# Kernel tuning notes

Hardware: AMD Instinct MI355X
Metric: run time of the kernel (lower is better)

## Reference

```python
import jax, jax.numpy as jnp
import numpy as np

FRAC_BIT = 12
SCALE = float(2 ** FRAC_BIT)          # 12 fractional bits
QMIN, QMAX = -32768.0, 32767.0        # signed 16-bit two's complement range


def quant16(x):
    """Quantize to signed 16-bit fixed point with 12 fractional bits.

    Matches float_to_16bits_tensor / bit_slice semantics: the bit-serial
    crossbar MVM of the sliced operands equals an exact integer product of
    these fixed-point values, rescaled back to float.
    """
    return jnp.clip(jnp.round(x * SCALE), QMIN, QMAX) / SCALE


def setup_inputs() -> dict:
    key = jax.random.key(0)
    k1, k2 = jax.random.split(key)
    x = jax.random.normal(k1, (32, 128, 56, 56), dtype=jnp.float32)
    # kaiming-ish scale so weights are well inside the fixed-point range
    weight = jax.random.normal(k2, (256, 128, 3, 3), dtype=jnp.float32) * 0.05
    return {"x": x, "weight": weight}


def reference(x, weight):
    # The nested i/j loop in the original slides a stride-1 window over the
    # zero-padded input, performing a bit-sliced crossbar MVM per pixel.
    # That is exactly conv2d(stride=1, padding=1) on 16-bit fixed-point
    # quantized input and weight (bias row in the crossbar is zero / unused).
    qx = quant16(x)
    qw = quant16(weight)
    out = jax.lax.conv_general_dilated(
        qx, qw,
        window_strides=(1, 1),
        padding=((1, 1), (1, 1)),
        dimension_numbers=("NCHW", "OIHW", "NCHW"),
    )
    return out
```

## Files before the change

kernel.cpp:

```cpp
#include <hip/hip_runtime.h>
#include <cstdint>
#include <cstddef>


typedef __attribute__((ext_vector_type(8))) short short8;
typedef __attribute__((ext_vector_type(4))) float floatx4;

#define NIMG 32
#define CIN  128
#define HW   56
#define KOUT 256
#define HP   58
#define XPAD_ELEMS ((size_t)NIMG * HP * HP * CIN)
#define WT_OFF_BYTES (XPAD_ELEMS * 2)
#define KK 1152

__device__ __forceinline__ uint16_t quant_bf16(float v) {
    float q = rintf(v * 4096.0f);
    q = fminf(fmaxf(q, -32768.0f), 32767.0f) * (1.0f / 4096.0f);
    union { float f; uint32_t u; } cv; cv.f = q;
    uint32_t u = cv.u;
    return (uint16_t)((u + 0x7fffu + ((u >> 16) & 1u)) >> 16);
}

__global__ __launch_bounds__(256) void quant_pad_x(const float* __restrict__ x,
                                                   uint16_t* __restrict__ xp) {
    const int b = blockIdx.x;
    const int n = b / HP, hp = b - n * HP;
    uint16_t* row = xp + (size_t)(n * HP + hp) * HP * CIN;

    if (hp == 0 || hp == HP - 1) {
        uint4 z{0, 0, 0, 0};
        uint4* d = (uint4*)row;
        for (int t = threadIdx.x; t < HP * CIN * 2 / 16; t += 256) d[t] = z;
        return;
    }
    const int h = hp - 1;
    __shared__ uint16_t tile[HW * 130];
    const float* src = x + (size_t)n * CIN * HW * HW + (size_t)h * HW;
    for (int t = threadIdx.x; t < CIN * 14; t += 256) {
        int c = t / 14, w4 = t - c * 14;
        float4 v = *(const float4*)(src + (size_t)c * (HW * HW) + w4 * 4);
        int base = (w4 * 4) * 130 + c;
        tile[base]       = quant_bf16(v.x);
        tile[base + 130] = quant_bf16(v.y);
        tile[base + 260] = quant_bf16(v.z);
        tile[base + 390] = quant_bf16(v.w);
    }
    __syncthreads();
    if (threadIdx.x < 32) {
        uint4 z{0, 0, 0, 0};
        if (threadIdx.x < 16) ((uint4*)row)[threadIdx.x] = z;
        else ((uint4*)(row + 57 * CIN))[threadIdx.x - 16] = z;
    }
    uint2* dst = (uint2*)(row + CIN);
    for (int t = threadIdx.x; t < (HW * CIN) / 4; t += 256) {
        int w = t >> 5, c4 = (t & 31) * 4;
        uint32_t a = tile[w * 130 + c4]     | ((uint32_t)tile[w * 130 + c4 + 1] << 16);
        uint32_t c = tile[w * 130 + c4 + 2] | ((uint32_t)tile[w * 130 + c4 + 3] << 16);
        dst[t] = make_uint2(a, c);
    }
}

__global__ __launch_bounds__(256) void quant_w(const float* __restrict__ w,
                                               uint16_t* __restrict__ wt) {
    int i = blockIdx.x * 256 + threadIdx.x;
    int k = i / KK;
    int r = i - k * KK;
    int tap = r >> 7;
    int c = r & 127;
    wt[i] = quant_bf16(w[(size_t)(k * CIN + c) * 9 + tap]);
}

__global__ __launch_bounds__(256) void conv_gemm(const uint16_t* __restrict__ xp,
                                                 const uint16_t* __restrict__ wt,
                                                 float* __restrict__ out) {
    __shared__ __align__(16) uint16_t As[128 * 64];
    __shared__ __align__(16) uint16_t Bs[128 * 64];

    const int tid = threadIdx.x;
    const int l   = tid & 63;
    const int wv  = tid >> 6;
    const int wr  = wv >> 1;
    const int wc  = wv & 1;
    const int kblk  = blockIdx.x;
    const int pxblk = blockIdx.y;

    const int srow   = l >> 3;
    const int c_data = (l & 7) ^ srow;

    const uint16_t* aG[4];
    const uint16_t* bG[4];
#pragma unroll
    for (int i = 0; i < 4; ++i) {
        int row = wv * 32 + i * 8 + srow;
        aG[i] = wt + (size_t)(kblk * 128 + row) * KK + c_data * 8;
        int p = pxblk * 128 + row;
        int n = p / 3136; int rem = p - n * 3136;
        int hh = rem / HW; int ww = rem - hh * HW;
        bG[i] = xp + (size_t)((n * HP + hh) * HP + ww) * CIN + c_data * 8;
    }

    floatx4 acc[4][4];
#pragma unroll
    for (int a = 0; a < 4; ++a)
#pragma unroll
        for (int b = 0; b < 4; ++b)
            acc[a][b] = (floatx4){0.f, 0.f, 0.f, 0.f};

    const int m16 = l & 15;
    const int q   = l >> 4;
    const int r7  = m16 & 7;

    for (int tap = 0; tap < 9; ++tap) {
        const int toff = ((tap / 3) * HP + (tap % 3)) * CIN;
#pragma unroll
        for (int c64 = 0; c64 < 2; ++c64) {
            const int koff = tap * 128 + c64 * 64;
#pragma unroll
            for (int i = 0; i < 4; ++i) {
                __builtin_amdgcn_global_load_lds(
                    (__attribute__((address_space(1))) void*)(void*)(aG[i] + koff),
                    (__attribute__((address_space(3))) void*)(void*)(&As[(wv * 32 + i * 8) * 64]),
                    16, 0, 0);
                __builtin_amdgcn_global_load_lds(
                    (__attribute__((address_space(1))) void*)(void*)(bG[i] + toff + c64 * 64),
                    (__attribute__((address_space(3))) void*)(void*)(&Bs[(wv * 32 + i * 8) * 64]),
                    16, 0, 0);
            }
            __syncthreads();
#pragma unroll
            for (int s = 0; s < 2; ++s) {
                const int slot = ((s * 4 + q) ^ r7) * 8;
                short8 af[4], bf[4];
#pragma unroll
                for (int f = 0; f < 4; ++f) {
                    af[f] = *(const short8*)&As[(wr * 64 + f * 16 + m16) * 64 + slot];
                    bf[f] = *(const short8*)&Bs[(wc * 64 + f * 16 + m16) * 64 + slot];
                }
#pragma unroll
                for (int fr = 0; fr < 4; ++fr)
#pragma unroll
                    for (int fc = 0; fc < 4; ++fc)
                        acc[fr][fc] = __builtin_amdgcn_mfma_f32_16x16x32_bf16(
                            af[fr], bf[fc], acc[fr][fc], 0, 0, 0);
            }
            __syncthreads();
        }
    }

#pragma unroll
    for (int fc = 0; fc < 4; ++fc) {
        int p = pxblk * 128 + wc * 64 + fc * 16 + m16;
        int n = p / 3136; int rem = p - n * 3136;
        float* op = out + (size_t)(n * KOUT + kblk * 128) * 3136 + rem;
#pragma unroll
        for (int fr = 0; fr < 4; ++fr) {
            int kl = wr * 64 + fr * 16 + q * 4;
#pragma unroll
            for (int t = 0; t < 4; ++t)
                op[(size_t)(kl + t) * 3136] = acc[fr][fc][t];
        }
    }
}

extern "C" void kernel_launch(void* const* d_in, const int* in_sizes, int n_in,
                              void* d_out, int out_size, void* d_ws, size_t ws_size,
                              hipStream_t stream) {
    const float* x = (const float*)d_in[0];
    const float* w = (const float*)d_in[1];
    float* out = (float*)d_out;

    uint16_t* xp  = (uint16_t*)d_ws;
    uint16_t* wtb = (uint16_t*)((char*)d_ws + WT_OFF_BYTES);

    quant_pad_x<<<NIMG * HP, 256, 0, stream>>>(x, xp);
    quant_w<<<(KOUT * KK) / 256, 256, 0, stream>>>(w, wtb);

    dim3 grid(2, 784);
    conv_gemm<<<grid, 256, 0, stream>>>(xp, wtb, out);
}
```

Measured before the change: 219.6 us.

## Rewrite conv GEMM as 256x256 tile with double-buffered LDS ping-pong pipeline

Replaces the 128x128 single-buffered tile (grid 2x784, 4 waves) with 256x256 tiles per block of 8 waves, double-buffered LDS, and async global-to-LDS prefetch two k-steps ahead. MFMA phases are split into quarters with barrier, setprio and sched_barrier interleaving, so loads overlap compute. Blocks are remapped across 8 groups of 49 to spread pixel tiles. The aim is to hide global load latency and improve data reuse. The cost is 128KB of LDS, higher register pressure, and only 392 blocks, which may underfill the CUs.

```diff
diff --git a/kernel.cpp b/kernel.cpp
--- a/kernel.cpp
+++ b/kernel.cpp
@@ -72,96 +72,187 @@
     wt[i] = quant_bf16(w[(size_t)(k * CIN + c) * 9 + tap]);
 }
 
-__global__ __launch_bounds__(256) void conv_gemm(const uint16_t* __restrict__ xp,
-                                                 const uint16_t* __restrict__ wt,
-                                                 float* __restrict__ out) {
-    __shared__ __align__(16) uint16_t As[128 * 64];
-    __shared__ __align__(16) uint16_t Bs[128 * 64];
-
-    const int tid = threadIdx.x;
-    const int l   = tid & 63;
-    const int wv  = tid >> 6;
-    const int wr  = wv >> 1;
-    const int wc  = wv & 1;
-    const int kblk  = blockIdx.x;
-    const int pxblk = blockIdx.y;
-
-    const int srow   = l >> 3;
+
+#define GLOAD(gsrc, ldst)                                                      \
+    __builtin_amdgcn_global_load_lds(                                          \
+        (__attribute__((address_space(1))) void*)(void*)(gsrc),                \
+        (__attribute__((address_space(3))) void*)(void*)(ldst), 16, 0, 0)
+
+#define STAGE_A(bsel, kt) do {                                                 \
+    GLOAD(aGp[0][0] + (size_t)(kt) * 64, &ldsA[bsel][0][(wv * 8) * 64]);       \
+    GLOAD(aGp[0][1] + (size_t)(kt) * 64, &ldsA[bsel][0][(64 + wv * 8) * 64]);  \
+    GLOAD(aGp[1][0] + (size_t)(kt) * 64, &ldsA[bsel][1][(wv * 8) * 64]);       \
+    GLOAD(aGp[1][1] + (size_t)(kt) * 64, &ldsA[bsel][1][(64 + wv * 8) * 64]);  \
+} while (0)
+
+#define STAGE_B(bsel, kt) do {                                                 \
+    const int tap_ = (kt) >> 1;                                                \
+    const size_t boff_ = (size_t)((tap_ / 3) * HP + (tap_ % 3)) * CIN          \
+                       + (size_t)((kt) & 1) * 64;                              \
+    GLOAD(bGp[0][0] + boff_, &ldsB[bsel][0][(wv * 8) * 64]);                   \
+    GLOAD(bGp[0][1] + boff_, &ldsB[bsel][0][(64 + wv * 8) * 64]);              \
+    GLOAD(bGp[1][0] + boff_, &ldsB[bsel][1][(wv * 8) * 64]);                   \
+    GLOAD(bGp[1][1] + boff_, &ldsB[bsel][1][(64 + wv * 8) * 64]);              \
+} while (0)
+
+#define READ_A(bsel, q4) do {                                                  \
+    _Pragma("unroll")                                                          \
+    for (int f_ = 0; f_ < 4; ++f_) {                                           \
+        const int r_ = (q4) * 64 + f_ * 16 + m16;                              \
+        ra[f_][0] = *(const short8*)&ldsA[bsel][wm][r_ * 64 + sl0];            \
+        ra[f_][1] = *(const short8*)&ldsA[bsel][wm][r_ * 64 + sl1];            \
+    }                                                                          \
+} while (0)
+
+#define READ_B(dst, bsel, ch) do {                                             \
+    _Pragma("unroll")                                                          \
+    for (int fc_ = 0; fc_ < 2; ++fc_) {                                        \
+        const int r_ = bl + (ch) * 32 + fc_ * 16 + m16;                        \
+        dst[fc_][0] = *(const short8*)&ldsB[bsel][bh][r_ * 64 + sl0];          \
+        dst[fc_][1] = *(const short8*)&ldsB[bsel][bh][r_ * 64 + sl1];          \
+    }                                                                          \
+} while (0)
+
+#define MFMA_Q(q4, ch, B) do {                                                 \
+    _Pragma("unroll")                                                          \
+    for (int s_ = 0; s_ < 2; ++s_)                                             \
+    _Pragma("unroll")                                                          \
+    for (int f_ = 0; f_ < 4; ++f_)                                             \
+    _Pragma("unroll")                                                          \
+    for (int c_ = 0; c_ < 2; ++c_)                                             \
+        acc[q4][f_][ch][c_] = __builtin_amdgcn_mfma_f32_16x16x32_bf16(         \
+            ra[f_][s_], B[c_][s_], acc[q4][f_][ch][c_], 0, 0, 0);              \
+} while (0)
+
+#define PHASE_TAIL(...) do {                                                   \
+    __builtin_amdgcn_s_barrier();                                              \
+    asm volatile("s_waitcnt lgkmcnt(0)" ::: "memory");                         \
+    __builtin_amdgcn_sched_barrier(0);                                         \
+    __builtin_amdgcn_s_setprio(1);                                             \
+    __VA_ARGS__;                                                               \
+    __builtin_amdgcn_s_setprio(0);                                             \
+    __builtin_amdgcn_s_barrier();                                              \
+} while (0)
+
+__global__ __launch_bounds__(512, 2) void conv_gemm(const uint16_t* __restrict__ xp,
+                                                    const uint16_t* __restrict__ wt,
+                                                    float* __restrict__ out) {
+    __shared__ __align__(16) uint16_t ldsA[2][2][128 * 64];
+    __shared__ __align__(16) uint16_t ldsB[2][2][128 * 64];
+
+    const int tid  = threadIdx.x;
+    const int l    = tid & 63;
+    const int wv   = tid >> 6;
+    const int wm   = wv >> 2;
+    const int wn   = wv & 3;
+    const int bh   = wn >> 1;
+    const int bl   = (wn & 1) * 64;
+    const int srow = l >> 3;
     const int c_data = (l & 7) ^ srow;
-
-    const uint16_t* aG[4];
-    const uint16_t* bG[4];
-#pragma unroll
-    for (int i = 0; i < 4; ++i) {
-        int row = wv * 32 + i * 8 + srow;
-        aG[i] = wt + (size_t)(kblk * 128 + row) * KK + c_data * 8;
-        int p = pxblk * 128 + row;
-        int n = p / 3136; int rem = p - n * 3136;
-        int hh = rem / HW; int ww = rem - hh * HW;
-        bG[i] = xp + (size_t)((n * HP + hh) * HP + ww) * CIN + c_data * 8;
-    }
-
-    floatx4 acc[4][4];
-#pragma unroll
-    for (int a = 0; a < 4; ++a)
-#pragma unroll
-        for (int b = 0; b < 4; ++b)
-            acc[a][b] = (floatx4){0.f, 0.f, 0.f, 0.f};
-
-    const int m16 = l & 15;
-    const int q   = l >> 4;
-    const int r7  = m16 & 7;
-
-    for (int tap = 0; tap < 9; ++tap) {
-        const int toff = ((tap / 3) * HP + (tap % 3)) * CIN;
-#pragma unroll
-        for (int c64 = 0; c64 < 2; ++c64) {
-            const int koff = tap * 128 + c64 * 64;
-#pragma unroll
-            for (int i = 0; i < 4; ++i) {
-                __builtin_amdgcn_global_load_lds(
-                    (__attribute__((address_space(1))) void*)(void*)(aG[i] + koff),
-                    (__attribute__((address_space(3))) void*)(void*)(&As[(wv * 32 + i * 8) * 64]),
-                    16, 0, 0);
-                __builtin_amdgcn_global_load_lds(
-                    (__attribute__((address_space(1))) void*)(void*)(bG[i] + toff + c64 * 64),
-                    (__attribute__((address_space(3))) void*)(void*)(&Bs[(wv * 32 + i * 8) * 64]),
-                    16, 0, 0);
-            }
-            __syncthreads();
-#pragma unroll
-            for (int s = 0; s < 2; ++s) {
-                const int slot = ((s * 4 + q) ^ r7) * 8;
-                short8 af[4], bf[4];
+    const int m16  = l & 15;
+    const int q    = l >> 4;
+    const int r7   = m16 & 7;
+    const int sl0  = ((0 + q) ^ r7) * 8;
+    const int sl1  = ((4 + q) ^ r7) * 8;
+
+    const int b = blockIdx.x;
+    const int pxblk = (b & 7) * 49 + (b >> 3);
+
+    const uint16_t* aGp[2][2];
+    const uint16_t* bGp[2][2];
+#pragma unroll
+    for (int h_ = 0; h_ < 2; ++h_)
+#pragma unroll
+        for (int j_ = 0; j_ < 2; ++j_) {
+            const int row = h_ * 128 + j_ * 64 + wv * 8 + srow;
+            aGp[h_][j_] = wt + (size_t)row * KK + c_data * 8;
+            const int p = pxblk * 256 + row;
+            const int n = p / 3136; const int rem = p - n * 3136;
+            const int hh = rem / HW; const int ww = rem - hh * HW;
+            bGp[h_][j_] = xp + (size_t)((n * HP + hh) * HP + ww) * CIN + c_data * 8;
+        }
+
+    floatx4 acc[2][4][2][2];
+#pragma unroll
+    for (int a_ = 0; a_ < 2; ++a_)
+#pragma unroll
+        for (int f_ = 0; f_ < 4; ++f_)
+#pragma unroll
+            for (int c_ = 0; c_ < 2; ++c_)
+#pragma unroll
+                for (int d_ = 0; d_ < 2; ++d_)
+                    acc[a_][f_][c_][d_] = (floatx4){0.f, 0.f, 0.f, 0.f};
+
+    short8 ra[4][2];
+    short8 rb0[2][2];
+    short8 rb1[2][2];
+
+    STAGE_A(0, 0); STAGE_B(0, 0);
+    STAGE_A(1, 1); STAGE_B(1, 1);
+    asm volatile("s_waitcnt vmcnt(8)" ::: "memory");
+    __builtin_amdgcn_s_barrier();
+
+#pragma unroll 1
+    for (int it = 0; it < 8; ++it) {
+        const int ktE = 2 * it + 2;
+        const int ktO = 2 * it + 3;
+        READ_A(0, 0);
+        READ_B(rb0, 0, 0);
+        PHASE_TAIL(MFMA_Q(0, 0, rb0));
+        READ_B(rb1, 0, 1);
+        PHASE_TAIL(MFMA_Q(0, 1, rb1));
+        READ_A(0, 1);
+        PHASE_TAIL(MFMA_Q(1, 0, rb0));
+        STAGE_A(0, ktE); STAGE_B(0, ktE);
+        asm volatile("s_waitcnt vmcnt(8)" ::: "memory");
+        PHASE_TAIL(MFMA_Q(1, 1, rb1));
+        READ_A(1, 0);
+        READ_B(rb0, 1, 0);
+        PHASE_TAIL(MFMA_Q(0, 0, rb0));
+        READ_B(rb1, 1, 1);
+        PHASE_TAIL(MFMA_Q(0, 1, rb1));
+        READ_A(1, 1);
+        PHASE_TAIL(MFMA_Q(1, 0, rb0));
+        STAGE_A(1, ktO); STAGE_B(1, ktO);
+        asm volatile("s_waitcnt vmcnt(8)" ::: "memory");
+        PHASE_TAIL(MFMA_Q(1, 1, rb1));
+    }
+
+    READ_A(0, 0);
+    READ_B(rb0, 0, 0);
+    PHASE_TAIL(MFMA_Q(0, 0, rb0));
+    READ_B(rb1, 0, 1);
+    PHASE_TAIL(MFMA_Q(0, 1, rb1));
+    READ_A(0, 1);
+    PHASE_TAIL(MFMA_Q(1, 0, rb0));
+    asm volatile("s_waitcnt vmcnt(0)" ::: "memory");
+    PHASE_TAIL(MFMA_Q(1, 1, rb1));
+    READ_A(1, 0);
+    READ_B(rb0, 1, 0);
+    PHASE_TAIL(MFMA_Q(0, 0, rb0));
+    READ_B(rb1, 1, 1);
+    PHASE_TAIL(MFMA_Q(0, 1, rb1));
+    READ_A(1, 1);
+    PHASE_TAIL(MFMA_Q(1, 0, rb0));
+    PHASE_TAIL(MFMA_Q(1, 1, rb1));
+
+#pragma unroll
+    for (int ch = 0; ch < 2; ++ch)
+#pragma unroll
+        for (int fc = 0; fc < 2; ++fc) {
+            const int p = pxblk * 256 + wn * 64 + ch * 32 + fc * 16 + m16;
+            const int n = p / 3136; const int rem = p - n * 3136;
+            float* op = out + (size_t)(n * KOUT + wm * 128) * 3136 + rem;
+#pragma unroll
+            for (int q4 = 0; q4 < 2; ++q4)
 #pragma unroll
                 for (int f = 0; f < 4; ++f) {
-                    af[f] = *(const short8*)&As[(wr * 64 + f * 16 + m16) * 64 + slot];
-                    bf[f] = *(const short8*)&Bs[(wc * 64 + f * 16 + m16) * 64 + slot];
+                    const int kl = q4 * 64 + f * 16 + q * 4;
+#pragma unroll
+                    for (int t = 0; t < 4; ++t)
+                        op[(size_t)(kl + t) * 3136] = acc[q4][f][ch][fc][t];
                 }
-#pragma unroll
-                for (int fr = 0; fr < 4; ++fr)
-#pragma unroll
-                    for (int fc = 0; fc < 4; ++fc)
-                        acc[fr][fc] = __builtin_amdgcn_mfma_f32_16x16x32_bf16(
-                            af[fr], bf[fc], acc[fr][fc], 0, 0, 0);
-            }
-            __syncthreads();
         }
-    }
-
-#pragma unroll
-    for (int fc = 0; fc < 4; ++fc) {
-        int p = pxblk * 128 + wc * 64 + fc * 16 + m16;
-        int n = p / 3136; int rem = p - n * 3136;
-        float* op = out + (size_t)(n * KOUT + kblk * 128) * 3136 + rem;
-#pragma unroll
-        for (int fr = 0; fr < 4; ++fr) {
-            int kl = wr * 64 + fr * 16 + q * 4;
-#pragma unroll
-            for (int t = 0; t < 4; ++t)
-                op[(size_t)(kl + t) * 3136] = acc[fr][fc][t];
-        }
-    }
 }
 
 extern "C" void kernel_launch(void* const* d_in, const int* in_sizes, int n_in,
@@ -177,6 +268,5 @@
     quant_pad_x<<<NIMG * HP, 256, 0, stream>>>(x, xp);
     quant_w<<<(KOUT * KK) / 256, 256, 0, stream>>>(w, wtb);
 
-    dim3 grid(2, 784);
-    conv_gemm<<<grid, 256, 0, stream>>>(xp, wtb, out);
-}
+    conv_gemm<<<dim3(392), dim3(512), 0, stream>>>(xp, wtb, out);
+}
```

After: 220.0 us. No clear change (+0.2%).
